# Kernel optimization log

Hardware: AMD Instinct MI355X
Metric: run time of the kernel (lower is better)

## Reference

```python
import jax, jax.numpy as jnp
import numpy as np

# layer dims: 30->24->19->14->10->6->2->1
_DIMS = [30, 24, 19, 14, 10, 6, 2, 1]


def setup_inputs() -> dict:
    key = jax.random.key(0)
    ks = jax.random.split(key, 1 + 2 * (len(_DIMS) - 1))
    inp = {"x": jax.random.normal(ks[0], (1048576, 30), dtype=jnp.float32)}
    for i in range(len(_DIMS) - 1):
        fan_in, fan_out = _DIMS[i], _DIMS[i + 1]
        bound = 1.0 / np.sqrt(fan_in)
        inp[f"W{i+1}"] = jax.random.uniform(ks[1 + 2 * i], (fan_out, fan_in), dtype=jnp.float32, minval=-bound, maxval=bound)
        inp[f"b{i+1}"] = jax.random.uniform(ks[2 + 2 * i], (fan_out,), dtype=jnp.float32, minval=-bound, maxval=bound)
    return inp


def reference(x, W1, b1, W2, b2, W3, b3, W4, b4, W5, b5, W6, b6, W7, b7):
    # 6 Linear+ReLU layers, then final Linear (no activation)
    for W, b in [(W1, b1), (W2, b2), (W3, b3), (W4, b4), (W5, b5), (W6, b6)]:
        x = jax.nn.relu(x @ W.T + b)
    return x @ W7.T + b7
```

## Files before the change

kernel.cpp:

```cpp
#include <hip/hip_runtime.h>


#define NTHREADS 256
#define TPW 4

typedef __fp16       h2     __attribute__((ext_vector_type(2)));
typedef __fp16       half8  __attribute__((ext_vector_type(8)));
typedef float        f32x16 __attribute__((ext_vector_type(16)));
typedef unsigned int uint4v __attribute__((ext_vector_type(4)));

__device__ __forceinline__ h2 cpk(float a, float b) {
    return __builtin_bit_cast(h2, __builtin_amdgcn_cvt_pkrtz(a, b));
}
__device__ __forceinline__ h2 relu2(h2 v) {
    h2 z = {(__fp16)0.f, (__fp16)0.f};
#if __has_builtin(__builtin_elementwise_max)
    return __builtin_elementwise_max(v, z);
#else
    v.x = v.x > (__fp16)0.f ? v.x : (__fp16)0.f;
    v.y = v.y > (__fp16)0.f ? v.y : (__fp16)0.f;
    return v;
#endif
}
__device__ __forceinline__ unsigned ucast(h2 v) { return __builtin_bit_cast(unsigned, v); }

__device__ __forceinline__ f32x16 mfma_(half8 A, half8 B, f32x16 C) {
    return __builtin_amdgcn_mfma_f32_32x32x16_f16(A, B, C, 0, 0, 0);
}

template <int FIN, int FOUT, int KPAD>
__device__ __forceinline__ void stageW(const float* __restrict__ W, const float* __restrict__ B,
                                       __fp16* __restrict__ sbase, int t) {
    for (int idx = t; idx < 32 * KPAD; idx += NTHREADS) {
        int m = idx / KPAD;
        int k = idx & (KPAD - 1);
        float v = 0.f;
        if (m < FOUT) {
            if (k < FIN) v = W[m * FIN + k];
            else if (k == FIN) v = B[m];
        }
        int byte = idx * 2;
        byte ^= (m & 7) << 4;
        *(__fp16*)((char*)sbase + byte) = (__fp16)v;
    }
}

__device__ __forceinline__ half8 ldA(const __fp16* base, int KPAD, int ks, int lane) {
    int m = lane & 31;
    int byte = (m * KPAD + ks * 16 + ((lane >> 5) & 1) * 8) * 2;
    byte ^= (m & 7) << 4;
    return __builtin_bit_cast(half8, *(const uint4v*)((const char*)base + byte));
}

template <int R, int POS>
__device__ __forceinline__ half8 bfrag(const f32x16& d, int lane) {
    unsigned u0 = ucast(relu2(cpk(d[R + 0], d[R + 1])));
    unsigned u1 = ucast(relu2(cpk(d[R + 2], d[R + 3])));
    unsigned u2 = ucast(relu2(cpk(d[R + 4], d[R + 5])));
    unsigned u3 = ucast(relu2(cpk(d[R + 6], d[R + 7])));
    bool lo = (lane & 32) == 0;
    unsigned s0 = __shfl_xor(u0, 32), s1 = __shfl_xor(u1, 32);
    unsigned s2 = __shfl_xor(u2, 32), s3 = __shfl_xor(u3, 32);
    unsigned w0 = lo ? u0 : s2;
    unsigned w1 = lo ? u1 : s3;
    unsigned w2 = lo ? s0 : u2;
    unsigned w3 = lo ? s1 : u3;
    if constexpr (POS >= 0) {
        constexpr bool hiT = POS >= 8;
        constexpr int  p   = POS & 7;
        constexpr unsigned bits = (p & 1) ? 0x3C000000u : 0x00003C00u;
        bool sel = (((lane & 32) != 0) == hiT);
        unsigned ob = sel ? bits : 0u;
        if constexpr ((p >> 1) == 0) w0 |= ob;
        else if constexpr ((p >> 1) == 1) w1 |= ob;
        else if constexpr ((p >> 1) == 2) w2 |= ob;
        else w3 |= ob;
    }
    uint4v u = {w0, w1, w2, w3};
    return __builtin_bit_cast(half8, u);
}

__device__ __forceinline__ half8 packx(unsigned a, unsigned b, unsigned c, unsigned d) {
    uint4v u = {a, b, c, d};
    return __builtin_bit_cast(half8, u);
}

__global__ __launch_bounds__(NTHREADS, 3) void mlp_mfma3(
    const float* __restrict__ x,
    const float* __restrict__ W1, const float* __restrict__ B1,
    const float* __restrict__ W2, const float* __restrict__ B2,
    const float* __restrict__ W3, const float* __restrict__ B3,
    const float* __restrict__ W4, const float* __restrict__ B4,
    const float* __restrict__ W5, const float* __restrict__ B5,
    const float* __restrict__ W6, const float* __restrict__ B6,
    const float* __restrict__ W7, const float* __restrict__ B7,
    float* __restrict__ out, int nrows)
{
    __shared__ __align__(16) __fp16 shw[5120];
    __shared__ __align__(16) float  sxw[4][960];

    const int t    = threadIdx.x;
    const int lane = t & 63;
    const int wid  = t >> 6;
    const int hb   = (lane >> 5) & 1;

    stageW<30, 24, 32>(W1, B1, shw + 0,    t);
    stageW<24, 19, 32>(W2, B2, shw + 1024, t);
    stageW<19, 14, 32>(W3, B3, shw + 2048, t);
    stageW<14, 10, 16>(W4, B4, shw + 3072, t);
    stageW<10, 6,  16>(W5, B5, shw + 3584, t);
    stageW<6,  2,  16>(W6, B6, shw + 4096, t);
    stageW<2,  1,  16>(W7, B7, shw + 4608, t);
    __syncthreads();

    const half8 A10 = ldA(shw + 0,    32, 0, lane), A11 = ldA(shw + 0,    32, 1, lane);
    const half8 A20 = ldA(shw + 1024, 32, 0, lane), A21 = ldA(shw + 1024, 32, 1, lane);
    const half8 A30 = ldA(shw + 2048, 32, 0, lane), A31 = ldA(shw + 2048, 32, 1, lane);
    const half8 A4  = ldA(shw + 3072, 16, 0, lane);
    const half8 A5  = ldA(shw + 3584, 16, 0, lane);
    const half8 A6  = ldA(shw + 4096, 16, 0, lane);
    const half8 A7  = ldA(shw + 4608, 16, 0, lane);

    const f32x16 z = {0.f,0.f,0.f,0.f, 0.f,0.f,0.f,0.f, 0.f,0.f,0.f,0.f, 0.f,0.f,0.f,0.f};

    const int tile0 = (blockIdx.x * 4 + wid) * TPW;
    float4* wb = (float4*)sxw[wid];

    float4 pf0, pf1, pf2, pf3;
    {
        const float4* gx = (const float4*)x + (size_t)tile0 * 240;
        pf0 = gx[lane];
        pf1 = gx[lane + 64];
        pf2 = gx[lane + 128];
        if (lane < 48) pf3 = gx[lane + 192];
    }

    for (int it = 0; it < TPW; ++it) {
        const int T = tile0 + it;

        wb[lane]       = pf0;
        wb[lane + 64]  = pf1;
        wb[lane + 128] = pf2;
        if (lane < 48) wb[lane + 192] = pf3;

        const float* xr = sxw[wid] + (lane & 31) * 30;
        float f0a[8], f1a[8];
        {
            const float2* p0 = (const float2*)(xr + hb * 8);
            float2 a = p0[0], b = p0[1], c = p0[2], d = p0[3];
            f0a[0] = a.x; f0a[1] = a.y; f0a[2] = b.x; f0a[3] = b.y;
            f0a[4] = c.x; f0a[5] = c.y; f0a[6] = d.x; f0a[7] = d.y;
            const float2* p1 = (const float2*)(xr + 16 + hb * 8);
            float2 e = p1[0], g = p1[1], h = p1[2], i = p1[3];
            f1a[0] = e.x; f1a[1] = e.y; f1a[2] = g.x; f1a[3] = g.y;
            f1a[4] = h.x; f1a[5] = h.y; f1a[6] = i.x; f1a[7] = i.y;
        }
        half8 Bx0 = packx(ucast(cpk(f0a[0], f0a[1])), ucast(cpk(f0a[2], f0a[3])),
                          ucast(cpk(f0a[4], f0a[5])), ucast(cpk(f0a[6], f0a[7])));
        unsigned x13 = hb ? 0x00003C00u : ucast(cpk(f1a[6], f1a[7]));
        half8 Bx1 = packx(ucast(cpk(f1a[0], f1a[1])), ucast(cpk(f1a[2], f1a[3])),
                          ucast(cpk(f1a[4], f1a[5])), x13);

        if (it + 1 < TPW) {
            const float4* gx = (const float4*)x + (size_t)(T + 1) * 240;
            pf0 = gx[lane];
            pf1 = gx[lane + 64];
            pf2 = gx[lane + 128];
            if (lane < 48) pf3 = gx[lane + 192];
        }

        f32x16 a1 = mfma_(A10, Bx0, z);
        a1 = mfma_(A11, Bx1, a1);
        f32x16 a2 = mfma_(A20, bfrag<0, -1>(a1, lane), z);
        a2 = mfma_(A21, bfrag<8, 8>(a1, lane), a2);
        f32x16 a3 = mfma_(A30, bfrag<0, -1>(a2, lane), z);
        a3 = mfma_(A31, bfrag<8, 3>(a2, lane), a3);
        f32x16 a4 = mfma_(A4, bfrag<0, 14>(a3, lane), z);
        f32x16 a5 = mfma_(A5, bfrag<0, 10>(a4, lane), z);
        f32x16 a6 = mfma_(A6, bfrag<0, 6>(a5, lane), z);
        f32x16 a7 = mfma_(A7, bfrag<0, 2>(a6, lane), z);

        const int row0 = T * 32;
        if (lane < 32) {
            int r = row0 + lane;
            if (r < nrows) out[r] = a7[0];
        }
    }
}

extern "C" void kernel_launch(void* const* d_in, const int* in_sizes, int n_in,
                              void* d_out, int out_size, void* d_ws, size_t ws_size,
                              hipStream_t stream) {
    const float* x = (const float*)d_in[0];
    int nrows = in_sizes[0] / 30;
    int rows_per_block = 4 * TPW * 32;
    int blocks = (nrows + rows_per_block - 1) / rows_per_block;
    mlp_mfma3<<<blocks, NTHREADS, 0, stream>>>(
        x,
        (const float*)d_in[1],  (const float*)d_in[2],
        (const float*)d_in[3],  (const float*)d_in[4],
        (const float*)d_in[5],  (const float*)d_in[6],
        (const float*)d_in[7],  (const float*)d_in[8],
        (const float*)d_in[9],  (const float*)d_in[10],
        (const float*)d_in[11], (const float*)d_in[12],
        (const float*)d_in[13], (const float*)d_in[14],
        (float*)d_out, nrows);
}
```

Measured before the change: 35.47 us.

## Load MFMA input fragments directly from global memory, drop LDS staging

Removes the per-wave LDS staging buffer for input rows; each lane now loads its own row's float2 fragments straight from global memory into registers and packs them into MFMA B operands. Tiles per wave are doubled and launch bounds are raised to 4 blocks per CU, which cuts block count and removes the LDS write/read round trip. The trade-off is strided, less coalesced global loads (each lane reads separate 8-byte pieces of a 120-byte row) and more register pressure from eight prefetch registers.

```diff
diff --git a/kernel.cpp b/kernel.cpp
--- a/kernel.cpp
+++ b/kernel.cpp
@@ -2,7 +2,7 @@
 
 
 #define NTHREADS 256
-#define TPW 4
+#define TPW 8
 
 typedef __fp16       h2     __attribute__((ext_vector_type(2)));
 typedef __fp16       half8  __attribute__((ext_vector_type(8)));
@@ -85,7 +85,7 @@
     return __builtin_bit_cast(half8, u);
 }
 
-__global__ __launch_bounds__(NTHREADS, 3) void mlp_mfma3(
+__global__ __launch_bounds__(NTHREADS, 4) void mlp_mfma4(
     const float* __restrict__ x,
     const float* __restrict__ W1, const float* __restrict__ B1,
     const float* __restrict__ W2, const float* __restrict__ B2,
@@ -97,7 +97,6 @@
     float* __restrict__ out, int nrows)
 {
     __shared__ __align__(16) __fp16 shw[5120];
-    __shared__ __align__(16) float  sxw[4][960];
 
     const int t    = threadIdx.x;
     const int lane = t & 63;
@@ -124,49 +123,42 @@
     const f32x16 z = {0.f,0.f,0.f,0.f, 0.f,0.f,0.f,0.f, 0.f,0.f,0.f,0.f, 0.f,0.f,0.f,0.f};
 
     const int tile0 = (blockIdx.x * 4 + wid) * TPW;
-    float4* wb = (float4*)sxw[wid];
-
-    float4 pf0, pf1, pf2, pf3;
+    const int myrow = lane & 31;
+
+    float2 pf0, pf1, pf2, pf3, pf4, pf5, pf6, pf7;
     {
-        const float4* gx = (const float4*)x + (size_t)tile0 * 240;
-        pf0 = gx[lane];
-        pf1 = gx[lane + 64];
-        pf2 = gx[lane + 128];
-        if (lane < 48) pf3 = gx[lane + 192];
+        const float* b0 = x + ((size_t)(tile0 * 32 + myrow)) * 30 + hb * 8;
+        pf0 = *(const float2*)(b0 + 0);
+        pf1 = *(const float2*)(b0 + 2);
+        pf2 = *(const float2*)(b0 + 4);
+        pf3 = *(const float2*)(b0 + 6);
+        const float* b1 = b0 + 16;
+        pf4 = *(const float2*)(b1 + 0);
+        pf5 = *(const float2*)(b1 + 2);
+        pf6 = *(const float2*)(b1 + 4);
+        if (!hb) pf7 = *(const float2*)(b1 + 6);
     }
 
     for (int it = 0; it < TPW; ++it) {
         const int T = tile0 + it;
 
-        wb[lane]       = pf0;
-        wb[lane + 64]  = pf1;
-        wb[lane + 128] = pf2;
-        if (lane < 48) wb[lane + 192] = pf3;
-
-        const float* xr = sxw[wid] + (lane & 31) * 30;
-        float f0a[8], f1a[8];
-        {
-            const float2* p0 = (const float2*)(xr + hb * 8);
-            float2 a = p0[0], b = p0[1], c = p0[2], d = p0[3];
-            f0a[0] = a.x; f0a[1] = a.y; f0a[2] = b.x; f0a[3] = b.y;
-            f0a[4] = c.x; f0a[5] = c.y; f0a[6] = d.x; f0a[7] = d.y;
-            const float2* p1 = (const float2*)(xr + 16 + hb * 8);
-            float2 e = p1[0], g = p1[1], h = p1[2], i = p1[3];
-            f1a[0] = e.x; f1a[1] = e.y; f1a[2] = g.x; f1a[3] = g.y;
-            f1a[4] = h.x; f1a[5] = h.y; f1a[6] = i.x; f1a[7] = i.y;
-        }
-        half8 Bx0 = packx(ucast(cpk(f0a[0], f0a[1])), ucast(cpk(f0a[2], f0a[3])),
-                          ucast(cpk(f0a[4], f0a[5])), ucast(cpk(f0a[6], f0a[7])));
-        unsigned x13 = hb ? 0x00003C00u : ucast(cpk(f1a[6], f1a[7]));
-        half8 Bx1 = packx(ucast(cpk(f1a[0], f1a[1])), ucast(cpk(f1a[2], f1a[3])),
-                          ucast(cpk(f1a[4], f1a[5])), x13);
+        half8 Bx0 = packx(ucast(cpk(pf0.x, pf0.y)), ucast(cpk(pf1.x, pf1.y)),
+                          ucast(cpk(pf2.x, pf2.y)), ucast(cpk(pf3.x, pf3.y)));
+        unsigned xlast = hb ? 0x00003C00u : ucast(cpk(pf7.x, pf7.y));
+        half8 Bx1 = packx(ucast(cpk(pf4.x, pf4.y)), ucast(cpk(pf5.x, pf5.y)),
+                          ucast(cpk(pf6.x, pf6.y)), xlast);
 
         if (it + 1 < TPW) {
-            const float4* gx = (const float4*)x + (size_t)(T + 1) * 240;
-            pf0 = gx[lane];
-            pf1 = gx[lane + 64];
-            pf2 = gx[lane + 128];
-            if (lane < 48) pf3 = gx[lane + 192];
+            const float* b0 = x + ((size_t)((T + 1) * 32 + myrow)) * 30 + hb * 8;
+            pf0 = *(const float2*)(b0 + 0);
+            pf1 = *(const float2*)(b0 + 2);
+            pf2 = *(const float2*)(b0 + 4);
+            pf3 = *(const float2*)(b0 + 6);
+            const float* b1 = b0 + 16;
+            pf4 = *(const float2*)(b1 + 0);
+            pf5 = *(const float2*)(b1 + 2);
+            pf6 = *(const float2*)(b1 + 4);
+            if (!hb) pf7 = *(const float2*)(b1 + 6);
         }
 
         f32x16 a1 = mfma_(A10, Bx0, z);
@@ -195,7 +187,7 @@
     int nrows = in_sizes[0] / 30;
     int rows_per_block = 4 * TPW * 32;
     int blocks = (nrows + rows_per_block - 1) / rows_per_block;
-    mlp_mfma3<<<blocks, NTHREADS, 0, stream>>>(
+    mlp_mfma4<<<blocks, NTHREADS, 0, stream>>>(
         x,
         (const float*)d_in[1],  (const float*)d_in[2],
         (const float*)d_in[3],  (const float*)d_in[4],
```

Result: faster. 31.32 us (-11.7%).
